# Optimization experiments

Hardware: AMD Instinct MI355X
Metric: run time of the kernel (lower is better)

## Reference

```python
import jax, jax.numpy as jnp
import numpy as np

BN_EPS = 1e-5

def batchnorm2d(x, gamma, beta):
    # x: [B, H, *, *]; normalize over (B, dim2, dim3) per channel H (training-mode batch stats)
    mean = jnp.mean(x, axis=(0, 2, 3), keepdims=True)
    var = jnp.var(x, axis=(0, 2, 3), keepdims=True)
    xhat = (x - mean) * jax.lax.rsqrt(var + BN_EPS)
    return xhat * gamma[None, :, None, None] + beta[None, :, None, None]

def setup_inputs() -> dict:
    key = jax.random.key(0)
    ks = jax.random.split(key, 8)
    B, N, C = 64, 196, 768
    H = 12
    hd = C // H  # 64
    patch = 196  # img_size**2, must equal N
    x = jax.random.normal(ks[0], (B, N, C), dtype=jnp.float32)
    W_qv = jax.random.normal(ks[1], (C, 2 * C), dtype=jnp.float32) * (1.0 / np.sqrt(C))
    k_ext = jax.random.normal(ks[2], (patch, hd), dtype=jnp.float32)  # torch init: ones; randomized for testing
    attn_bias = jax.random.normal(ks[3], (1, patch), dtype=jnp.float32) * 0.02
    bn_gamma = jnp.ones((H,), dtype=jnp.float32) + 0.1 * jax.random.normal(ks[4], (H,), dtype=jnp.float32)
    bn_beta = 0.1 * jax.random.normal(ks[5], (H,), dtype=jnp.float32)
    W_proj = jax.random.normal(ks[6], (C, C), dtype=jnp.float32) * (1.0 / np.sqrt(C))
    b_proj = jnp.zeros((C,), dtype=jnp.float32)
    return {"x": x, "W_qv": W_qv, "k_ext": k_ext, "attn_bias": attn_bias,
            "bn_gamma": bn_gamma, "bn_beta": bn_beta, "W_proj": W_proj, "b_proj": b_proj}

def reference(x, W_qv, k_ext, attn_bias, bn_gamma, bn_beta, W_proj, b_proj):
    B, N, C = x.shape
    H = bn_gamma.shape[0]
    hd = C // H
    scale = hd ** -0.5
    # qv projection: [B,N,2C] -> q,v each [B,H,N,hd]
    qv = (x @ W_qv).reshape(B, N, 2, H, hd).transpose(2, 0, 3, 1, 4)
    q, v = qv[0], qv[1]
    # scores against fixed k_ext: [B,H,N,patch]
    attn = jnp.einsum('bhnd,pd->bhnp', q, k_ext)
    attn = (batchnorm2d(attn, bn_gamma, bn_beta) + attn_bias) * scale
    attn = jax.nn.softmax(attn, axis=-1)
    v = batchnorm2d(v, bn_gamma, bn_beta)
    out = jnp.einsum('bhnp,bhpd->bhnd', attn, v)  # patch == N
    out = out.transpose(0, 2, 1, 3).reshape(B, N, C)
    return out @ W_proj + b_proj
```

## Files before the change

### kernel.cpp

```cpp
#include <hip/hip_runtime.h>
#include <hip/hip_bf16.h>

typedef __bf16 b16;
typedef __bf16 b16x4 __attribute__((ext_vector_type(4)));
typedef __bf16 b16x8 __attribute__((ext_vector_type(8)));
typedef float  f32x4 __attribute__((ext_vector_type(4)));

#define B_   64
#define N_   196
#define C_   768
#define H_   12
#define HD_  64
#define TOK  (B_*N_)
#define SCALE 0.125f

__device__ __forceinline__ void gl_lds16(const void* g, void* l){
  __builtin_amdgcn_global_load_lds((const __attribute__((address_space(1))) void*)g,
                                   (__attribute__((address_space(3))) void*)l, 16, 0, 0);
}

__global__ __launch_bounds__(256) void k_transpose_cvt(const float* __restrict__ in,
                                                       b16* __restrict__ out, int R, int C){
  __shared__ b16 tile[32][33];
  int tx = threadIdx.x, ty = threadIdx.y;
  int bx = blockIdx.x, by = blockIdx.y;
  int c = bx*32 + tx;
  #pragma unroll
  for (int i = 0; i < 32; i += 8){
    int r = by*32 + ty + i;
    tile[ty+i][tx] = (b16)in[(long)r*C + c];
  }
  __syncthreads();
  int rr = by*32 + tx;
  #pragma unroll
  for (int i = 0; i < 32; i += 8){
    int cc = bx*32 + ty + i;
    out[(long)cc*R + rr] = tile[tx][ty+i];
  }
}

__global__ __launch_bounds__(256) void k_cvt(const float* __restrict__ in, b16* __restrict__ out){
  long i = ((long)blockIdx.x*256 + threadIdx.x)*8;
  const float4* s = (const float4*)(in + i);
  float4 f0 = s[0], f1 = s[1];
  b16x8 v; v[0]=(b16)f0.x; v[1]=(b16)f0.y; v[2]=(b16)f0.z; v[3]=(b16)f0.w;
           v[4]=(b16)f1.x; v[5]=(b16)f1.y; v[6]=(b16)f1.z; v[7]=(b16)f1.w;
  *(b16x8*)(out + i) = v;
}

__global__ __launch_bounds__(256) void k_kprep(const float* __restrict__ k_ext,
                                               float* __restrict__ Kmat, float* __restrict__ ksum){
  __shared__ float ks[N_][HD_];
  int tid = threadIdx.x, blk = blockIdx.x;
  for (int i = tid; i < N_*HD_; i += 256) ks[i/HD_][i%HD_] = k_ext[i];
  __syncthreads();
  int i = tid >> 2;
  int j0 = blk*16 + (tid & 3)*4;
  float a0=0.f, a1=0.f, a2=0.f, a3=0.f;
  for (int p = 0; p < N_; ++p){
    float ki = ks[p][i];
    float4 kv = *(const float4*)&ks[p][j0];
    a0 += ki*kv.x; a1 += ki*kv.y; a2 += ki*kv.z; a3 += ki*kv.w;
  }
  Kmat[i*64+j0+0]=a0; Kmat[i*64+j0+1]=a1; Kmat[i*64+j0+2]=a2; Kmat[i*64+j0+3]=a3;
  if (blk == 0 && tid < 64){
    float s = 0.f;
    for (int p = 0; p < N_; ++p) s += ks[p][tid];
    ksum[tid] = s;
  }
}

template<int MODE>
__global__ __launch_bounds__(512, 2) void k_gemm(const b16* __restrict__ A,
                                                 const b16* __restrict__ BT,
                                                 b16* __restrict__ qout, b16* __restrict__ vout,
                                                 float* __restrict__ fout, const float* __restrict__ bias,
                                                 const float* __restrict__ ksum, float* __restrict__ stats){
  const int NT  = (MODE == 0) ? 6 : 3;
  const int NWG = 49*NT;
  int orig = blockIdx.x;
  int q8 = NWG >> 3, r8 = NWG & 7;
  int xcd = orig & 7, loc = orig >> 3;
  int bid = (xcd < r8 ? xcd*(q8+1) : r8*(q8+1) + (xcd-r8)*q8) + loc;
  int rt = bid / NT, ct = bid % NT;
  int brow = rt*256, bcol = ct*256;

  __shared__ char smc[2*32768];
  int tid = threadIdx.x, lane = tid & 63, w = tid >> 6;
  int wr = w >> 2, wc = w & 3;

  int gsrc = (lane & 3) ^ ((lane >> 3) & 3);
  const b16* gA = A  + (long)(brow + w*16 + (lane>>2))*768 + gsrc*8;
  const b16* gB = BT + (long)(bcol + w*16 + (lane>>2))*768 + gsrc*8;

#define STAGE(cur, t) do{ \
    char* ba = smc + (cur)*32768; \
    gl_lds16(gA + (long)(t)*32,           ba + (w*16)*64); \
    gl_lds16(gA + (long)(t)*32 + 128*768, ba + (128 + w*16)*64); \
    gl_lds16(gB + (long)(t)*32,           ba + 16384 + (w*16)*64); \
    gl_lds16(gB + (long)(t)*32 + 128*768, ba + 16384 + (128 + w*16)*64); \
  } while(0)

#define COMPUTE(cur) do{ \
    const char* ba = smc + (cur)*32768; \
    const char* bb = ba + 16384; \
    b16x8 af[8], bf[4]; \
    _Pragma("unroll") \
    for (int m = 0; m < 8; ++m){ \
      int row = wr*128 + m*16 + (lane & 15); \
      af[m] = *(const b16x8*)(ba + row*64 + (((lane>>4) ^ ((row>>1)&3))<<4)); \
    } \
    _Pragma("unroll") \
    for (int n = 0; n < 4; ++n){ \
      int row = wc*64 + n*16 + (lane & 15); \
      bf[n] = *(const b16x8*)(bb + row*64 + (((lane>>4) ^ ((row>>1)&3))<<4)); \
    } \
    _Pragma("unroll") \
    for (int m = 0; m < 8; ++m) \
      _Pragma("unroll") \
      for (int n = 0; n < 4; ++n) \
        acc[m][n] = __builtin_amdgcn_mfma_f32_16x16x32_bf16(bf[n], af[m], acc[m][n], 0, 0, 0); \
  } while(0)

  f32x4 acc[8][4];
  #pragma unroll
  for (int m = 0; m < 8; ++m)
    #pragma unroll
    for (int n = 0; n < 4; ++n) acc[m][n] = (f32x4){0.f,0.f,0.f,0.f};

  STAGE(0, 0);
  STAGE(1, 1);

  #pragma unroll 1
  for (int kt = 0; kt < 23; ++kt){
    int cur = kt & 1;
    asm volatile("s_waitcnt vmcnt(4)" ::: "memory");
    __builtin_amdgcn_s_barrier();
    asm volatile("" ::: "memory");
    COMPUTE(cur);
    asm volatile("s_waitcnt lgkmcnt(0)" ::: "memory");
    __builtin_amdgcn_s_barrier();
    asm volatile("" ::: "memory");
    if (kt < 22) STAGE(cur, kt+2);
  }
  asm volatile("s_waitcnt vmcnt(0)" ::: "memory");
  __builtin_amdgcn_s_barrier();
  asm volatile("" ::: "memory");
  COMPUTE(1);
#undef COMPUTE
#undef STAGE

  if constexpr (MODE == 0){
    int hidx = ct*4 + wc;
    bool isV = (hidx >= 12);
    b16* dst = isV ? vout : qout;
    int cb0 = bcol + wc*64 - (isV ? 768 : 0);
    #pragma unroll
    for (int m = 0; m < 8; ++m){
      int r2 = brow + wr*128 + m*16 + (lane & 15);
      #pragma unroll
      for (int n = 0; n < 4; ++n){
        int cc = cb0 + n*16 + ((lane>>4)<<2);
        b16x4 pv;
        #pragma unroll
        for (int j = 0; j < 4; ++j) pv[j] = (b16)acc[m][n][j];
        *(b16x4*)(dst + (long)r2*768 + cc) = pv;
      }
    }
    {
      float a_acc = 0.f, b_acc = 0.f;
      #pragma unroll
      for (int n = 0; n < 4; ++n)
        #pragma unroll
        for (int j = 0; j < 4; ++j){
          int d = n*16 + ((lane>>4)<<2) + j;
          float s = 0.f, s2 = 0.f;
          #pragma unroll
          for (int m = 0; m < 8; ++m){
            float v = acc[m][n][j];
            s += v; s2 += v*v;
          }
          if (isV){ a_acc += s; b_acc += s2; }
          else      a_acc += s * ksum[d];
        }
      #pragma unroll
      for (int off = 1; off < 64; off <<= 1){
        a_acc += __shfl_xor(a_acc, off, 64);
        b_acc += __shfl_xor(b_acc, off, 64);
      }
      if (lane == 0){
        if (isV){
          atomicAdd(&stats[24 + (hidx-12)], a_acc);
          atomicAdd(&stats[36 + (hidx-12)], b_acc);
        } else {
          atomicAdd(&stats[hidx], a_acc);
        }
      }
    }
  } else {
    #pragma unroll
    for (int m = 0; m < 8; ++m){
      int r2 = brow + wr*128 + m*16 + (lane & 15);
      #pragma unroll
      for (int n = 0; n < 4; ++n){
        int cc = bcol + wc*64 + n*16 + ((lane>>4)<<2);
        f32x4 bv = *(const f32x4*)(bias + cc);
        f32x4 o;
        #pragma unroll
        for (int j = 0; j < 4; ++j) o[j] = acc[m][n][j] + bv[j];
        *(f32x4*)(fout + (long)r2*768 + cc) = o;
      }
    }
  }
}

__global__ __launch_bounds__(256) void k_gram(const b16* __restrict__ qb, float* __restrict__ G){
  __shared__ b16 qT[64*232];
  int tid = threadIdx.x, lane = tid & 63, w = tid >> 6;
  int h = blockIdx.x % 12, bg = blockIdx.x / 12;
  f32x4 acc[4];
  #pragma unroll
  for (int n = 0; n < 4; ++n) acc[n] = (f32x4){0.f,0.f,0.f,0.f};
  #pragma unroll 1
  for (int r = 0; r < 2; ++r){
    int b = bg*2 + r;
    const b16* src = qb + (long)(b*196)*768 + h*64;
    int d = lane;
    for (int p0 = w*8; p0 < 224; p0 += 32){
      b16x8 w8;
      #pragma unroll
      for (int j = 0; j < 8; ++j){
        int p = p0 + j;
        w8[j] = (p < 196) ? src[(long)p*768 + d] : (b16)0.f;
      }
      *(b16x8*)(qT + d*232 + p0) = w8;
    }
    __syncthreads();
    #pragma unroll
    for (int ks = 0; ks < 7; ++ks){
      int t0 = ks*32;
      b16x8 af = *(const b16x8*)(qT + (16*w + (lane&15))*232 + t0 + ((lane>>4)<<3));
      #pragma unroll
      for (int n = 0; n < 4; ++n){
        b16x8 bf = *(const b16x8*)(qT + (16*n + (lane&15))*232 + t0 + ((lane>>4)<<3));
        acc[n] = __builtin_amdgcn_mfma_f32_16x16x32_bf16(af, bf, acc[n], 0, 0, 0);
      }
    }
    __syncthreads();
  }
  float* Gh = G + h*4096;
  #pragma unroll
  for (int n = 0; n < 4; ++n)
    #pragma unroll
    for (int j = 0; j < 4; ++j){
      int i  = 16*w + ((lane>>4)<<2) + j;
      int jj = 16*n + (lane&15);
      atomicAdd(&Gh[i*64 + jj], acc[n][j]);
    }
}

__global__ __launch_bounds__(256) void k_sfin(const float* __restrict__ G, const float* __restrict__ Kmat,
                                              const float* __restrict__ stats, const float* __restrict__ gamma,
                                              const float* __restrict__ beta, float* __restrict__ coef){
  int h = blockIdx.x, tid = threadIdx.x;
  const float* Gh = G + h*4096;
  float s = 0.f;
  #pragma unroll
  for (int k = 0; k < 16; ++k) s += Gh[tid + k*256]*Kmat[tid + k*256];
  #pragma unroll
  for (int off = 1; off < 64; off <<= 1) s += __shfl_xor(s, off, 64);
  __shared__ float red[4];
  if ((tid & 63) == 0) red[tid>>6] = s;
  __syncthreads();
  if (tid == 0){
    float S2 = red[0]+red[1]+red[2]+red[3];
    const float cntS = 2458624.f, cntV = 802816.f;
    float S1 = stats[h], VS = stats[24+h], VS2 = stats[36+h];
    float ms = S1/cntS;
    float vars = S2/cntS - ms*ms;
    float alpha = gamma[h]*SCALE*rsqrtf(vars + 1e-5f);
    float mv = VS/cntV;
    float varv = VS2/cntV - mv*mv;
    float a = gamma[h]*rsqrtf(varv + 1e-5f);
    coef[h*4+0] = alpha;
    coef[h*4+1] = a;
    coef[h*4+2] = beta[h] - a*mv;
  }
}

__global__ __launch_bounds__(256, 2) void k_attn(const b16* __restrict__ qb, const b16* __restrict__ vb,
                                                 const float* __restrict__ k_ext,
                                                 const float* __restrict__ attn_bias,
                                                 const float* __restrict__ coef,
                                                 b16* __restrict__ Ob){
  __shared__ b16 ksh[196*64];
  __shared__ b16 vsh[64*216];
  __shared__ b16 psh[4][16*200];
  __shared__ float bsh[196];

  int tid = threadIdx.x, lane = tid & 63, wid = tid >> 6;
  int bh = blockIdx.x;
  int h = bh % 12, b = bh / 12;
  const b16* qt = qb + (long)(b*196)*768 + h*64;
  const b16* vt = vb + (long)(b*196)*768 + h*64;
  float alpha = coef[h*4+0], av = coef[h*4+1], cv = coef[h*4+2];

  for (int c = tid; c < 196*8; c += 256){
    int p = c >> 3, g = c & 7;
    const float4* src = (const float4*)(k_ext + p*64 + g*8);
    float4 f0 = src[0], f1 = src[1];
    b16x8 v; v[0]=(b16)f0.x; v[1]=(b16)f0.y; v[2]=(b16)f0.z; v[3]=(b16)f0.w;
             v[4]=(b16)f1.x; v[5]=(b16)f1.y; v[6]=(b16)f1.z; v[7]=(b16)f1.w;
    *(b16x8*)((char*)ksh + p*128 + ((g ^ (p&7))<<4)) = v;
  }
  for (int p = tid; p < 196; p += 256) bsh[p] = attn_bias[p]*SCALE;
  {
    int d = tid & 63;
    for (int p0 = (tid>>6)*8; p0 < 196; p0 += 32){
      b16x8 w;
      #pragma unroll
      for (int j = 0; j < 8; ++j){
        int p = p0 + j;
        w[j] = (p < 196) ? vt[(long)p*768 + d] : (b16)0.f;
      }
      *(b16x8*)((char*)vsh + d*432 + p0*2) = w;
    }
  }
  __syncthreads();

  for (int rt = wid; rt < 13; rt += 4){
    int n0 = rt*16;
    int qrow = n0 + (lane & 15); if (qrow > 195) qrow = 195;
    b16x8 a0 = *(const b16x8*)((const char*)qt + (long)qrow*1536 +      ((lane>>4)<<4));
    b16x8 a1 = *(const b16x8*)((const char*)qt + (long)qrow*1536 + 64 + ((lane>>4)<<4));

    f32x4 sc[13];
    #pragma unroll
    for (int ct = 0; ct < 13; ++ct){
      int p = ct*16 + (lane & 15); int pc = p > 195 ? 195 : p;
      b16x8 b0 = *(const b16x8*)((const char*)ksh + pc*128 + ((( (lane>>4))   ^ (pc&7))<<4));
      b16x8 b1 = *(const b16x8*)((const char*)ksh + pc*128 + (((4+(lane>>4))  ^ (pc&7))<<4));
      f32x4 z = {0.f,0.f,0.f,0.f};
      z = __builtin_amdgcn_mfma_f32_16x16x32_bf16(a0, b0, z, 0, 0, 0);
      z = __builtin_amdgcn_mfma_f32_16x16x32_bf16(a1, b1, z, 0, 0, 0);
      sc[ct] = z;
    }
    int pcol = lane & 15;
    float mx[4] = {-1e30f,-1e30f,-1e30f,-1e30f};
    #pragma unroll
    for (int ct = 0; ct < 13; ++ct){
      int p = ct*16 + pcol;
      bool valid = (p < 196);
      float badd = valid ? bsh[p < 196 ? p : 0] : 0.f;
      #pragma unroll
      for (int j = 0; j < 4; ++j){
        float lv = valid ? (sc[ct][j]*alpha + badd) : -1e30f;
        sc[ct][j] = lv;
        mx[j] = fmaxf(mx[j], lv);
      }
    }
    #pragma unroll
    for (int off = 1; off < 16; off <<= 1)
      #pragma unroll
      for (int j = 0; j < 4; ++j) mx[j] = fmaxf(mx[j], __shfl_xor(mx[j], off, 64));
    float sm[4] = {0.f,0.f,0.f,0.f};
    #pragma unroll
    for (int ct = 0; ct < 13; ++ct)
      #pragma unroll
      for (int j = 0; j < 4; ++j){
        float e = __expf(sc[ct][j] - mx[j]);
        sc[ct][j] = e; sm[j] += e;
      }
    #pragma unroll
    for (int off = 1; off < 16; off <<= 1)
      #pragma unroll
      for (int j = 0; j < 4; ++j) sm[j] += __shfl_xor(sm[j], off, 64);
    float rs[4];
    #pragma unroll
    for (int j = 0; j < 4; ++j) rs[j] = 1.f/sm[j];

    b16* pw = psh[wid];
    #pragma unroll
    for (int ct = 0; ct < 12; ++ct){
      int p = ct*16 + pcol;
      #pragma unroll
      for (int j = 0; j < 4; ++j){
        int r = ((lane>>4)<<2) + j;
        pw[r*200 + p] = (b16)(sc[ct][j]*rs[j]);
      }
    }
    float pt12[4];
    #pragma unroll
    for (int j = 0; j < 4; ++j) pt12[j] = sc[12][j]*rs[j];

    __asm__ volatile("s_waitcnt lgkmcnt(0)" ::: "memory");
    __builtin_amdgcn_sched_barrier(0);

    f32x4 o[4];
    #pragma unroll
    for (int dt = 0; dt < 4; ++dt) o[dt] = (f32x4){0.f,0.f,0.f,0.f};
    #pragma unroll
    for (int pt = 0; pt < 6; ++pt){
      b16x8 pa = *(const b16x8*)((const char*)pw + (lane&15)*400 + pt*64 + ((lane>>4)<<4));
      #pragma unroll
      for (int dt = 0; dt < 4; ++dt){
        b16x8 vf = *(const b16x8*)((const char*)vsh + (dt*16 + (lane&15))*432 + pt*64 + ((lane>>4)<<4));
        o[dt] = __builtin_amdgcn_mfma_f32_16x16x32_bf16(pa, vf, o[dt], 0, 0, 0);
      }
    }
    #pragma unroll
    for (int e = 0; e < 4; ++e){
      float pe[4];
      #pragma unroll
      for (int j = 0; j < 4; ++j) pe[j] = __shfl(pt12[j], (lane & 48) + e, 64);
      #pragma unroll
      for (int dt = 0; dt < 4; ++dt){
        b16 vv = *((const b16*)((const char*)vsh + (dt*16 + (lane&15))*432 + (192+e)*2));
        float vvf = (float)vv;
        #pragma unroll
        for (int j = 0; j < 4; ++j) o[dt][j] += pe[j]*vvf;
      }
    }
    #pragma unroll
    for (int dt = 0; dt < 4; ++dt)
      #pragma unroll
      for (int j = 0; j < 4; ++j){
        int n = n0 + ((lane>>4)<<2) + j;
        if (n < 196){
          long idx = ((long)(b*196 + n))*768 + h*64 + dt*16 + (lane&15);
          Ob[idx] = (b16)(av*o[dt][j] + cv);
        }
      }
  }
}

extern "C" void kernel_launch(void* const* d_in, const int* in_sizes, int n_in,
                              void* d_out, int out_size, void* d_ws, size_t ws_size,
                              hipStream_t stream){
  const float* x         = (const float*)d_in[0];
  const float* W_qv      = (const float*)d_in[1];
  const float* k_ext     = (const float*)d_in[2];
  const float* attn_bias = (const float*)d_in[3];
  const float* bn_gamma  = (const float*)d_in[4];
  const float* bn_beta   = (const float*)d_in[5];
  const float* W_proj    = (const float*)d_in[6];
  const float* b_proj    = (const float*)d_in[7];
  float* out = (float*)d_out;

  char* ws = (char*)d_ws;
  const long SZ = 19267584;
  b16*   q_buf   = (b16*)(ws);
  b16*   v_buf   = (b16*)(ws + SZ);
  b16*   O_buf   = (b16*)(ws + 2*SZ);
  b16*   x_bf16  = (b16*)(ws + 2*SZ);
  b16*   W_qvT   = (b16*)(ws + 3*SZ);
  b16*   W_projT = (b16*)(ws + 3*SZ + 2359296);
  float* Kmat    = (float*)(ws + 3*SZ + 3538944);
  float* ksum    = Kmat + 4096;
  float* stats   = ksum + 64;
  float* coef    = stats + 48;
  float* Ggram   = coef + 48;

  hipMemsetAsync(stats, 0, 48*sizeof(float), stream);
  hipMemsetAsync(Ggram, 0, 12*4096*sizeof(float), stream);

  dim3 tb(32, 8);
  k_transpose_cvt<<<dim3(1536/32, 768/32), tb, 0, stream>>>(W_qv,   W_qvT,   768, 1536);
  k_transpose_cvt<<<dim3(768/32,  768/32), tb, 0, stream>>>(W_proj, W_projT, 768, 768);
  k_cvt<<<4704, 256, 0, stream>>>(x, x_bf16);
  k_kprep<<<4, 256, 0, stream>>>(k_ext, Kmat, ksum);
  k_gemm<0><<<49*6, 512, 0, stream>>>(x_bf16, W_qvT, q_buf, v_buf, nullptr, nullptr, ksum, stats);
  k_gram<<<384, 256, 0, stream>>>(q_buf, Ggram);
  k_sfin<<<12, 256, 0, stream>>>(Ggram, Kmat, stats, bn_gamma, bn_beta, coef);
  k_attn<<<768, 256, 0, stream>>>(q_buf, v_buf, k_ext, attn_bias, coef, O_buf);
  k_gemm<1><<<49*3, 512, 0, stream>>>(O_buf, W_projT, nullptr, nullptr, out, b_proj, nullptr, nullptr);
}
```

Measured before the change: 194.6 us.

## Restructure GEMM mainloop with K=64 tiles, split A/B staging and interleaved loads

Both GEMMs now use 64-wide K tiles (12 iterations instead of 24) held in 128KB of dynamic LDS with separate double buffers for A and B, using an 8-way XOR swizzle. Global-to-LDS loads are spread across four sub-phases of each iteration and interleaved with the MFMA groups. Sched barriers and setprio are added to keep compute dense. The aim is to cut barrier count per K element and hide load latency better. The cost is 128KB of LDS per block, which likely drops occupancy to one 512-thread block per CU, and many extra barriers within each iteration.

```diff
diff --git a/kernel.cpp b/kernel.cpp
--- a/kernel.cpp
+++ b/kernel.cpp
@@ -85,41 +85,26 @@
   int rt = bid / NT, ct = bid % NT;
   int brow = rt*256, bcol = ct*256;
 
-  __shared__ char smc[2*32768];
+  extern __shared__ char smc[];
   int tid = threadIdx.x, lane = tid & 63, w = tid >> 6;
   int wr = w >> 2, wc = w & 3;
 
-  int gsrc = (lane & 3) ^ ((lane >> 3) & 3);
-  const b16* gA = A  + (long)(brow + w*16 + (lane>>2))*768 + gsrc*8;
-  const b16* gB = BT + (long)(bcol + w*16 + (lane>>2))*768 + gsrc*8;
-
-#define STAGE(cur, t) do{ \
-    char* ba = smc + (cur)*32768; \
-    gl_lds16(gA + (long)(t)*32,           ba + (w*16)*64); \
-    gl_lds16(gA + (long)(t)*32 + 128*768, ba + (128 + w*16)*64); \
-    gl_lds16(gB + (long)(t)*32,           ba + 16384 + (w*16)*64); \
-    gl_lds16(gB + (long)(t)*32 + 128*768, ba + 16384 + (128 + w*16)*64); \
+  int l8 = lane >> 3;
+  int g8 = (lane & 7) ^ (l8 & 7);
+  const b16* gA = A  + (long)(brow + w*16 + l8)*768 + g8*8;
+  const b16* gB = BT + (long)(bcol + w*16 + l8)*768 + g8*8;
+
+#define STA(tt, h) do{ \
+    char* dst = smc + (((tt)&1)*32768) + (h)*16384 + w*2048; \
+    const b16* src = gA + (long)(h)*98304 + (long)(tt)*64; \
+    gl_lds16(src,          dst); \
+    gl_lds16(src + 6144,   dst + 1024); \
   } while(0)
-
-#define COMPUTE(cur) do{ \
-    const char* ba = smc + (cur)*32768; \
-    const char* bb = ba + 16384; \
-    b16x8 af[8], bf[4]; \
-    _Pragma("unroll") \
-    for (int m = 0; m < 8; ++m){ \
-      int row = wr*128 + m*16 + (lane & 15); \
-      af[m] = *(const b16x8*)(ba + row*64 + (((lane>>4) ^ ((row>>1)&3))<<4)); \
-    } \
-    _Pragma("unroll") \
-    for (int n = 0; n < 4; ++n){ \
-      int row = wc*64 + n*16 + (lane & 15); \
-      bf[n] = *(const b16x8*)(bb + row*64 + (((lane>>4) ^ ((row>>1)&3))<<4)); \
-    } \
-    _Pragma("unroll") \
-    for (int m = 0; m < 8; ++m) \
-      _Pragma("unroll") \
-      for (int n = 0; n < 4; ++n) \
-        acc[m][n] = __builtin_amdgcn_mfma_f32_16x16x32_bf16(bf[n], af[m], acc[m][n], 0, 0, 0); \
+#define STB(tt, h) do{ \
+    char* dst = smc + 65536 + (((tt)&1)*32768) + (h)*16384 + w*2048; \
+    const b16* src = gB + (long)(h)*98304 + (long)(tt)*64; \
+    gl_lds16(src,          dst); \
+    gl_lds16(src + 6144,   dst + 1024); \
   } while(0)
 
   f32x4 acc[8][4];
@@ -128,27 +113,63 @@
     #pragma unroll
     for (int n = 0; n < 4; ++n) acc[m][n] = (f32x4){0.f,0.f,0.f,0.f};
 
-  STAGE(0, 0);
-  STAGE(1, 1);
-
-  #pragma unroll 1
-  for (int kt = 0; kt < 23; ++kt){
-    int cur = kt & 1;
-    asm volatile("s_waitcnt vmcnt(4)" ::: "memory");
-    __builtin_amdgcn_s_barrier();
-    asm volatile("" ::: "memory");
-    COMPUTE(cur);
-    asm volatile("s_waitcnt lgkmcnt(0)" ::: "memory");
-    __builtin_amdgcn_s_barrier();
-    asm volatile("" ::: "memory");
-    if (kt < 22) STAGE(cur, kt+2);
-  }
-  asm volatile("s_waitcnt vmcnt(0)" ::: "memory");
+  STA(0,0); STA(0,1); STB(0,0); STB(0,1); STB(1,0); STB(1,1);
+  asm volatile("s_waitcnt vmcnt(4)" ::: "memory");
   __builtin_amdgcn_s_barrier();
   asm volatile("" ::: "memory");
-  COMPUTE(1);
-#undef COMPUTE
-#undef STAGE
+
+  #pragma unroll 1
+  for (int t = 0; t < 12; ++t){
+    const char* abase = smc + (t&1)*32768 + wr*16384;
+    const char* bbase = smc + 65536 + (t&1)*32768 + (wc>>1)*16384 + (wc&1)*8192;
+    b16x8 bf[4][2];
+    #pragma unroll
+    for (int p = 0; p < 4; ++p){
+      b16x8 af[2][2];
+      #pragma unroll
+      for (int mp = 0; mp < 2; ++mp)
+        #pragma unroll
+        for (int kh = 0; kh < 2; ++kh)
+          af[mp][kh] = *(const b16x8*)(abase + ((2*p+mp)*16 + (lane&15))*128
+                                       + ((((kh<<2)+(lane>>4)) ^ (lane&7))<<4));
+      if (p == 0){
+        #pragma unroll
+        for (int n = 0; n < 4; ++n)
+          #pragma unroll
+          for (int kh = 0; kh < 2; ++kh)
+            bf[n][kh] = *(const b16x8*)(bbase + (n*16 + (lane&15))*128
+                                        + ((((kh<<2)+(lane>>4)) ^ (lane&7))<<4));
+      }
+      if (p == 0 && t < 11) STA(t+1, 0);
+      if (p == 1 && t < 11) STA(t+1, 1);
+      if (p == 2 && t < 10) STB(t+2, 0);
+      if (p == 3 && t < 10) STB(t+2, 1);
+      asm volatile("" ::: "memory");
+      __builtin_amdgcn_s_barrier();
+      asm volatile("s_waitcnt lgkmcnt(0)" ::: "memory");
+      __builtin_amdgcn_sched_barrier(0);
+      __builtin_amdgcn_s_setprio(1);
+      #pragma unroll
+      for (int mp = 0; mp < 2; ++mp)
+        #pragma unroll
+        for (int n = 0; n < 4; ++n)
+          #pragma unroll
+          for (int kh = 0; kh < 2; ++kh)
+            acc[2*p+mp][n] = __builtin_amdgcn_mfma_f32_16x16x32_bf16(bf[n][kh], af[mp][kh],
+                                                                     acc[2*p+mp][n], 0, 0, 0);
+      __builtin_amdgcn_s_setprio(0);
+      __builtin_amdgcn_sched_barrier(0);
+      if (p == 3){
+        if (t < 10)       asm volatile("s_waitcnt vmcnt(4)" ::: "memory");
+        else if (t == 10) asm volatile("s_waitcnt vmcnt(0)" ::: "memory");
+      }
+      asm volatile("" ::: "memory");
+      __builtin_amdgcn_s_barrier();
+      asm volatile("" ::: "memory");
+    }
+  }
+#undef STA
+#undef STB
 
   if constexpr (MODE == 0){
     int hidx = ct*4 + wc;
@@ -469,9 +490,9 @@
   k_transpose_cvt<<<dim3(768/32,  768/32), tb, 0, stream>>>(W_proj, W_projT, 768, 768);
   k_cvt<<<4704, 256, 0, stream>>>(x, x_bf16);
   k_kprep<<<4, 256, 0, stream>>>(k_ext, Kmat, ksum);
-  k_gemm<0><<<49*6, 512, 0, stream>>>(x_bf16, W_qvT, q_buf, v_buf, nullptr, nullptr, ksum, stats);
+  k_gemm<0><<<49*6, 512, 131072, stream>>>(x_bf16, W_qvT, q_buf, v_buf, nullptr, nullptr, ksum, stats);
   k_gram<<<384, 256, 0, stream>>>(q_buf, Ggram);
   k_sfin<<<12, 256, 0, stream>>>(Ggram, Kmat, stats, bn_gamma, bn_beta, coef);
   k_attn<<<768, 256, 0, stream>>>(q_buf, v_buf, k_ext, attn_bias, coef, O_buf);
-  k_gemm<1><<<49*3, 512, 0, stream>>>(O_buf, W_projT, nullptr, nullptr, out, b_proj, nullptr, nullptr);
-}
+  k_gemm<1><<<49*3, 512, 131072, stream>>>(O_buf, W_projT, nullptr, nullptr, out, b_proj, nullptr, nullptr);
+}
```

After: 196.7 us. No clear change (+1.1%).
